# Performance work log

Hardware: AMD Instinct MI355X
Metric: run time of the kernel (lower is better)

## Reference

```python
import jax, jax.numpy as jnp
import numpy as np

B, N, C, H = 2, 2048, 768, 12
HD = C // H  # head dim = 64


def setup_inputs() -> dict:
    key = jax.random.key(0)
    k1, k2, k3 = jax.random.split(key, 3)
    x = jax.random.normal(k1, (B, N, C), dtype=jnp.float32)
    w_qkv = jax.random.normal(k2, (C, 3 * C), dtype=jnp.float32) * (C ** -0.5)
    w_proj = jax.random.normal(k3, (C, C), dtype=jnp.float32) * (C ** -0.5)
    b_proj = jnp.zeros((C,), dtype=jnp.float32)
    return {"x": x, "w_qkv": w_qkv, "w_proj": w_proj, "b_proj": b_proj}


def reference(x, w_qkv, w_proj, b_proj):
    scale = HD ** -0.5
    # qkv projection: [B,N,3C] -> [3,B,H,N,HD]
    qkv = (x @ w_qkv).reshape(B, N, 3, H, HD).transpose(2, 0, 3, 1, 4)
    q, k, v = qkv[0], qkv[1], qkv[2]
    # explicit QK^T softmax V (materializes [B,H,N,N] scores, as in source)
    attn = jnp.einsum("bhqd,bhkd->bhqk", q, k) * scale
    attn = jax.nn.softmax(attn, axis=-1)
    out = jnp.einsum("bhqk,bhkd->bhqd", attn, v)
    out = out.transpose(0, 2, 1, 3).reshape(B, N, C)
    return out @ w_proj + b_proj
```

## Files before the change

kernel.cpp:

```cpp
#include <hip/hip_runtime.h>

#define C_DIM 768
#define NSEQ 2048
#define H_DIM 12
#define HD 64
#define M_ROWS 4096
#define KSPLIT 2

typedef float f32x4 __attribute__((ext_vector_type(4)));
typedef short bf16x8 __attribute__((ext_vector_type(8)));
typedef _Float16 f16x8 __attribute__((ext_vector_type(8)));
typedef _Float16 f16x4 __attribute__((ext_vector_type(4)));
typedef __fp16 fp16x2 __attribute__((ext_vector_type(2)));
typedef __fp16 fp16x4 __attribute__((ext_vector_type(4)));
typedef __fp16 fp16x8 __attribute__((ext_vector_type(8)));
typedef unsigned short u16;

#define MFMA_PV(a, b, c) __builtin_amdgcn_mfma_f32_16x16x16f16(a, b, c, 0, 0, 0)

typedef unsigned int __attribute__((address_space(1))) as1_uint;
typedef unsigned int __attribute__((address_space(3))) as3_uint;
__device__ __forceinline__ void dma16(const void* g, void* l) {
  __builtin_amdgcn_global_load_lds((const as1_uint*)g, (as3_uint*)l, 16, 0, 0);
}

__device__ __forceinline__ u16 f2bf(float f) {
  union { float f; unsigned u; } v; v.f = f;
  unsigned u = v.u + 0x7FFFu + ((v.u >> 16) & 1u);
  return (u16)(u >> 16);
}

__global__ __launch_bounds__(256) void prep_kernel(const float* __restrict__ x,
                                                   const float* __restrict__ wq,
                                                   const float* __restrict__ wp,
                                                   u16* __restrict__ x_bf,
                                                   u16* __restrict__ outq,
                                                   __fp16* __restrict__ outp) {
  if (blockIdx.z == 2) {
    const int n4 = M_ROWS * C_DIM / 4;
    int lb = blockIdx.y * 72 + blockIdx.x;
    int i0 = lb * 256 + threadIdx.x;
    {
      float4 v = ((const float4*)x)[i0];
      ushort4 o;
      o.x = f2bf(v.x); o.y = f2bf(v.y); o.z = f2bf(v.z); o.w = f2bf(v.w);
      ((ushort4*)x_bf)[i0] = o;
    }
    int i1 = i0 + 442368;
    if (i1 < n4) {
      float4 v = ((const float4*)x)[i1];
      ushort4 o;
      o.x = f2bf(v.x); o.y = f2bf(v.y); o.z = f2bf(v.z); o.w = f2bf(v.w);
      ((ushort4*)x_bf)[i1] = o;
    }
    return;
  }
  const int R = C_DIM;
  __shared__ float t[32][33];
  int tx = threadIdx.x & 31, ty = threadIdx.x >> 5;
  int c0 = blockIdx.x * 32, r0 = blockIdx.y * 32;
  if (blockIdx.z == 0) {
    const int Cc = 3 * C_DIM;
#pragma unroll
    for (int i = 0; i < 4; i++)
      t[ty + i * 8][tx] = wq[(size_t)(r0 + ty + i * 8) * Cc + c0 + tx];
    __syncthreads();
#pragma unroll
    for (int i = 0; i < 4; i++)
      outq[(size_t)(c0 + ty + i * 8) * R + r0 + tx] = f2bf(t[tx][ty + i * 8]);
  } else {
    if (blockIdx.x >= 24) return;
    const int Cc = C_DIM;
#pragma unroll
    for (int i = 0; i < 4; i++)
      t[ty + i * 8][tx] = wp[(size_t)(r0 + ty + i * 8) * Cc + c0 + tx];
    __syncthreads();
#pragma unroll
    for (int i = 0; i < 4; i++)
      outp[(size_t)(c0 + ty + i * 8) * R + r0 + tx] = (__fp16)t[tx][ty + i * 8];
  }
}

__device__ __forceinline__ void gemm_core_128_db(const u16* __restrict__ A,
                                                 const u16* __restrict__ BT,
                                                 int m0, int n0,
                                                 u16 (*la)[128 * 32], u16 (*lb)[128 * 32],
                                                 f32x4 acc[4][4]) {
  const int K = C_DIM;
  int tid = threadIdx.x, lane = tid & 63, wave = tid >> 6;
  int wm = (wave >> 1) * 64, wn = (wave & 1) * 64;
  int quad = lane >> 4, l16 = lane & 15;

  int r0 = wave * 16 + (lane >> 2);
  int sw = (((lane & 3) ^ (r0 & 3)) * 8);
  const u16* ga0 = A + (size_t)(m0 + r0) * K + sw;
  const u16* ga1 = A + (size_t)(m0 + r0 + 64) * K + sw;
  const u16* gb0 = BT + (size_t)(n0 + r0) * K + sw;
  const u16* gb1 = BT + (size_t)(n0 + r0 + 64) * K + sw;
  int ofs0 = wave * 16 * 32, ofs1 = ofs0 + 64 * 32;

  dma16(ga0, la[0] + ofs0);
  dma16(ga1, la[0] + ofs1);
  dma16(gb0, lb[0] + ofs0);
  dma16(gb1, lb[0] + ofs1);

  const int NT = K / 32;
  for (int kt = 0; kt < NT; kt++) {
    int cur = kt & 1, nxt = cur ^ 1;
    __syncthreads();
    if (kt < NT - 1) {
      int k0 = (kt + 1) * 32;
      dma16(ga0 + k0, la[nxt] + ofs0);
      dma16(ga1 + k0, la[nxt] + ofs1);
      dma16(gb0 + k0, lb[nxt] + ofs0);
      dma16(gb1 + k0, lb[nxt] + ofs1);
    }
    bf16x8 af[4], bfr[4];
#pragma unroll
    for (int mt = 0; mt < 4; mt++) {
      int r = wm + mt * 16 + l16;
      af[mt] = *(const bf16x8*)(la[cur] + r * 32 + ((quad ^ (r & 3)) * 8));
    }
#pragma unroll
    for (int nt = 0; nt < 4; nt++) {
      int r = wn + nt * 16 + l16;
      bfr[nt] = *(const bf16x8*)(lb[cur] + r * 32 + ((quad ^ (r & 3)) * 8));
    }
#pragma unroll
    for (int mt = 0; mt < 4; mt++)
#pragma unroll
      for (int nt = 0; nt < 4; nt++)
        acc[mt][nt] = __builtin_amdgcn_mfma_f32_16x16x32_bf16(af[mt], bfr[nt], acc[mt][nt], 0, 0, 0);
  }
}

#define Q_PRESCALE 0.18033688011112042f
__global__ __launch_bounds__(256) void gemm_qkv_kernel(const u16* __restrict__ A,
                                                       const u16* __restrict__ BT,
                                                       _Float16* __restrict__ qb,
                                                       _Float16* __restrict__ kb,
                                                       _Float16* __restrict__ vtb) {
  __shared__ __align__(16) u16 la[2][128 * 32];
  __shared__ __align__(16) u16 lb[2][128 * 32];
  f32x4 acc[4][4] = {};
  int m0 = blockIdx.x * 128, n0 = blockIdx.y * 128;
  gemm_core_128_db(A, BT, m0, n0, la, lb, acc);

  int lane = threadIdx.x & 63, wave = threadIdx.x >> 6;
  int wm = (wave >> 1) * 64, wn = (wave & 1) * 64;
  int quad = lane >> 4, l16 = lane & 15;
#pragma unroll
  for (int mt = 0; mt < 4; mt++) {
#pragma unroll
    for (int nt = 0; nt < 4; nt++) {
      int gn = n0 + wn + nt * 16 + l16;
      int which = gn / C_DIM;
      int cc = gn - which * C_DIM;
      int h = cc >> 6, d = cc & 63;
      int gm0 = m0 + wm + mt * 16 + quad * 4;
      int b = gm0 >> 11, n = gm0 & 2047;
      size_t bh = (size_t)(b * H_DIM + h);
      if (which == 2) {
        f16x4 hv;
#pragma unroll
        for (int r = 0; r < 4; r++) hv[r] = (_Float16)acc[mt][nt][r];
        *(f16x4*)(vtb + (bh * HD + d) * NSEQ + n) = hv;
      } else if (which == 0) {
#pragma unroll
        for (int r = 0; r < 4; r++)
          qb[(bh * NSEQ + n + r) * HD + d] = (_Float16)(acc[mt][nt][r] * Q_PRESCALE);
      } else {
#pragma unroll
        for (int r = 0; r < 4; r++)
          kb[(bh * NSEQ + n + r) * HD + d] = (_Float16)acc[mt][nt][r];
      }
    }
  }
}

__global__ __launch_bounds__(256) void gemm_proj_kernel(const __fp16* __restrict__ opart,
                                                        const float* __restrict__ lpart,
                                                        const u16* __restrict__ BT,
                                                        const float* __restrict__ bias,
                                                        float* __restrict__ out) {
  __shared__ __align__(16) u16 la[2][64 * 32];
  __shared__ __align__(16) u16 lb[2][128 * 32];
  int tid = threadIdx.x, lane = tid & 63, wave = tid >> 6;
  int quad = lane >> 4, l16 = lane & 15;
  int wm = (wave >> 1) * 32, wn = (wave & 1) * 64;
  int m0 = blockIdx.x * 64, n0 = blockIdx.y * 128;

  int r0 = wave * 16 + (lane >> 2);
  int swb = (((lane & 3) ^ (r0 & 3)) * 8);
  const u16* gb0 = BT + (size_t)(n0 + r0) * C_DIM + swb;
  const u16* gb1 = BT + (size_t)(n0 + r0 + 64) * C_DIM + swb;
  int ofsB0 = wave * 16 * 32, ofsB1 = ofsB0 + 64 * 32;

  int ar = r0, cj = lane & 3;
  int m = m0 + ar;
  int bb = m >> 11, q = m & 2047;
  const __fp16* ap0 = opart + (size_t)m * C_DIM + cj * 8;
  const __fp16* ap1 = ap0 + (size_t)M_ROWS * C_DIM;
  int wslotA = ar * 32 + ((cj ^ (ar & 3)) * 8);

  f32x4 acc[2][4] = {};

  union pk_t { fp16x2 h2[4]; uint4 v; };

  dma16(gb0, lb[0] + ofsB0);
  dma16(gb1, lb[0] + ofsB1);
  {
    fp16x8 p0 = *(const fp16x8*)ap0;
    fp16x8 p1 = *(const fp16x8*)ap1;
    float l = lpart[((size_t)bb * H_DIM + 0) * NSEQ + q] +
              lpart[((size_t)(H_DIM * 2 + bb * H_DIM + 0)) * NSEQ + q];
    float inv = 1.f / l;
    pk_t w;
#pragma unroll
    for (int j = 0; j < 4; j++)
      w.h2[j] = __builtin_amdgcn_cvt_pkrtz(((float)p0[2 * j] + (float)p1[2 * j]) * inv,
                                           ((float)p0[2 * j + 1] + (float)p1[2 * j + 1]) * inv);
    *(uint4*)(la[0] + wslotA) = w.v;
  }

  const int NT = C_DIM / 32;
  for (int kt = 0; kt < NT; kt++) {
    int cur = kt & 1, nxt = cur ^ 1;
    __syncthreads();
    fp16x8 p0, p1;
    float inv = 0.f;
    if (kt < NT - 1) {
      int k0 = (kt + 1) * 32;
      dma16(gb0 + k0, lb[nxt] + ofsB0);
      dma16(gb1 + k0, lb[nxt] + ofsB1);
      p0 = *(const fp16x8*)(ap0 + k0);
      p1 = *(const fp16x8*)(ap1 + k0);
      int h = (kt + 1) >> 1;
      float l = lpart[((size_t)bb * H_DIM + h) * NSEQ + q] +
                lpart[((size_t)(H_DIM * 2 + bb * H_DIM + h)) * NSEQ + q];
      inv = 1.f / l;
    }
    f16x8 af[2], bf[4];
#pragma unroll
    for (int mt = 0; mt < 2; mt++) {
      int r = wm + mt * 16 + l16;
      af[mt] = *(const f16x8*)(la[cur] + r * 32 + ((quad ^ (r & 3)) * 8));
    }
#pragma unroll
    for (int nt = 0; nt < 4; nt++) {
      int r = wn + nt * 16 + l16;
      bf[nt] = *(const f16x8*)(lb[cur] + r * 32 + ((quad ^ (r & 3)) * 8));
    }
#pragma unroll
    for (int mt = 0; mt < 2; mt++)
#pragma unroll
      for (int nt = 0; nt < 4; nt++)
        acc[mt][nt] = __builtin_amdgcn_mfma_f32_16x16x32_f16(af[mt], bf[nt], acc[mt][nt], 0, 0, 0);
    if (kt < NT - 1) {
      pk_t w;
#pragma unroll
      for (int j = 0; j < 4; j++)
        w.h2[j] = __builtin_amdgcn_cvt_pkrtz(((float)p0[2 * j] + (float)p1[2 * j]) * inv,
                                             ((float)p0[2 * j + 1] + (float)p1[2 * j + 1]) * inv);
      *(uint4*)(la[nxt] + wslotA) = w.v;
    }
  }

#pragma unroll
  for (int mt = 0; mt < 2; mt++) {
#pragma unroll
    for (int nt = 0; nt < 4; nt++) {
      int gn = n0 + wn + nt * 16 + l16;
      float bv = bias[gn];
#pragma unroll
      for (int r = 0; r < 4; r++) {
        int gm = m0 + wm + mt * 16 + quad * 4 + r;
        out[(size_t)gm * C_DIM + gn] = acc[mt][nt][r] + bv;
      }
    }
  }
}

__global__ __launch_bounds__(256) void attn_kernel(const _Float16* __restrict__ qb,
                                                   const _Float16* __restrict__ kb,
                                                   const _Float16* __restrict__ vtb,
                                                   __fp16* __restrict__ opart,
                                                   float* __restrict__ lpart) {
  __shared__ __align__(16) u16 lk[2][64 * 72];
  __shared__ __align__(16) u16 lv[2][64 * 72];
  int bh = blockIdx.y, qblk = blockIdx.x, ks = blockIdx.z;
  int tid = threadIdx.x, lane = tid & 63, wave = tid >> 6;
  int quad = lane >> 4, l16 = lane & 15;

  const _Float16* q_bh = qb + (size_t)bh * NSEQ * HD;
  const u16* k_bh = (const u16*)(kb + (size_t)bh * NSEQ * HD);
  const u16* v_bh = (const u16*)(vtb + (size_t)bh * HD * NSEQ);

  int q0 = qblk * 128 + wave * 32 + l16;
  f16x8 qf[2][2];
#pragma unroll
  for (int qt = 0; qt < 2; qt++) {
    const _Float16* qp = q_bh + (size_t)(q0 + qt * 16) * HD + quad * 8;
    qf[qt][0] = *(const f16x8*)qp;
    qf[qt][1] = *(const f16x8*)(qp + 32);
  }

  f32x4 o[2][4] = {};
  float l_i[2] = {0.f, 0.f};

  int srow = tid >> 3, scj = tid & 7;
  const u16* kp0 = k_bh + (size_t)srow * HD + scj * 8;
  const u16* kp1 = kp0 + (size_t)32 * HD;
  const u16* vp0 = v_bh + (size_t)srow * NSEQ + scj * 8;
  const u16* vp1 = vp0 + (size_t)32 * NSEQ;
  int w0 = srow * 72 + scj * 8, w1 = (srow + 32) * 72 + scj * 8;

  const int kt_beg = ks * (NSEQ / 64 / KSPLIT);
  const int kt_end = kt_beg + (NSEQ / 64 / KSPLIT);

  {
    int k0 = kt_beg * 64;
    *(uint4*)(lk[0] + w0) = *(const uint4*)(kp0 + (size_t)k0 * HD);
    *(uint4*)(lk[0] + w1) = *(const uint4*)(kp1 + (size_t)k0 * HD);
    *(uint4*)(lv[0] + w0) = *(const uint4*)(vp0 + k0);
    *(uint4*)(lv[0] + w1) = *(const uint4*)(vp1 + k0);
  }

  for (int kt = kt_beg; kt < kt_end; kt++) {
    int cur = kt & 1, nxt = cur ^ 1;
    __syncthreads();

    uint4 rk0, rk1, rv0, rv1;
    if (kt < kt_end - 1) {
      int k0 = (kt + 1) * 64;
      rk0 = *(const uint4*)(kp0 + (size_t)k0 * HD);
      rk1 = *(const uint4*)(kp1 + (size_t)k0 * HD);
      rv0 = *(const uint4*)(vp0 + k0);
      rv1 = *(const uint4*)(vp1 + k0);
    }

    f32x4 s0[4], s1[4];
#pragma unroll
    for (int nt = 0; nt < 4; nt++) {
      const u16* kp = lk[cur] + (nt * 16 + l16) * 72 + quad * 8;
      f16x8 kf0 = *(const f16x8*)kp;
      f16x8 kf1 = *(const f16x8*)(kp + 32);
      f32x4 t0 = {}, t1 = {};
      t0 = __builtin_amdgcn_mfma_f32_16x16x32_f16(kf0, qf[0][0], t0, 0, 0, 0);
      t0 = __builtin_amdgcn_mfma_f32_16x16x32_f16(kf1, qf[0][1], t0, 0, 0, 0);
      t1 = __builtin_amdgcn_mfma_f32_16x16x32_f16(kf0, qf[1][0], t1, 0, 0, 0);
      t1 = __builtin_amdgcn_mfma_f32_16x16x32_f16(kf1, qf[1][1], t1, 0, 0, 0);
      s0[nt] = t0; s1[nt] = t1;
    }

#pragma unroll
    for (int nt = 0; nt < 4; nt++) {
      float a0 = __builtin_amdgcn_exp2f(s0[nt][0]);
      float a1 = __builtin_amdgcn_exp2f(s0[nt][1]);
      float a2 = __builtin_amdgcn_exp2f(s0[nt][2]);
      float a3 = __builtin_amdgcn_exp2f(s0[nt][3]);
      l_i[0] += (a0 + a1) + (a2 + a3);
      float b0 = __builtin_amdgcn_exp2f(s1[nt][0]);
      float b1 = __builtin_amdgcn_exp2f(s1[nt][1]);
      float b2 = __builtin_amdgcn_exp2f(s1[nt][2]);
      float b3 = __builtin_amdgcn_exp2f(s1[nt][3]);
      l_i[1] += (b0 + b1) + (b2 + b3);
      union { fp16x2 h2[2]; f16x4 h4; } pa, pb;
      pa.h2[0] = __builtin_amdgcn_cvt_pkrtz(a0, a1);
      pa.h2[1] = __builtin_amdgcn_cvt_pkrtz(a2, a3);
      pb.h2[0] = __builtin_amdgcn_cvt_pkrtz(b0, b1);
      pb.h2[1] = __builtin_amdgcn_cvt_pkrtz(b2, b3);
#pragma unroll
      for (int dt = 0; dt < 4; dt++) {
        f16x4 vf = *(const f16x4*)(lv[cur] + (dt * 16 + l16) * 72 + nt * 16 + quad * 4);
        o[0][dt] = MFMA_PV(vf, pa.h4, o[0][dt]);
        o[1][dt] = MFMA_PV(vf, pb.h4, o[1][dt]);
      }
    }

    if (kt < kt_end - 1) {
      *(uint4*)(lk[nxt] + w0) = rk0;
      *(uint4*)(lk[nxt] + w1) = rk1;
      *(uint4*)(lv[nxt] + w0) = rv0;
      *(uint4*)(lv[nxt] + w1) = rv1;
    }
  }

#pragma unroll
  for (int qt = 0; qt < 2; qt++) {
    l_i[qt] += __shfl_xor(l_i[qt], 16);
    l_i[qt] += __shfl_xor(l_i[qt], 32);
  }

  int b = bh / H_DIM, h = bh % H_DIM;
  __fp16* obase = opart + (size_t)ks * M_ROWS * C_DIM;
  float* lrow = lpart + ((size_t)ks * H_DIM * 2 + bh) * NSEQ;
#pragma unroll
  for (int qt = 0; qt < 2; qt++) {
    int q = q0 + qt * 16;
    if (quad == 0) lrow[q] = l_i[qt];
    __fp16* orow = obase + (size_t)(b * NSEQ + q) * C_DIM + h * HD;
#pragma unroll
    for (int dt = 0; dt < 4; dt++) {
      union { fp16x2 h2[2]; fp16x4 h4; } ov;
      ov.h2[0] = __builtin_amdgcn_cvt_pkrtz(o[qt][dt][0], o[qt][dt][1]);
      ov.h2[1] = __builtin_amdgcn_cvt_pkrtz(o[qt][dt][2], o[qt][dt][3]);
      *(fp16x4*)(orow + dt * 16 + quad * 4) = ov.h4;
    }
  }
}

extern "C" void kernel_launch(void* const* d_in, const int* in_sizes, int n_in,
                              void* d_out, int out_size, void* d_ws, size_t ws_size,
                              hipStream_t stream) {
  const float* x = (const float*)d_in[0];
  const float* w_qkv = (const float*)d_in[1];
  const float* w_proj = (const float*)d_in[2];
  const float* b_proj = (const float*)d_in[3];
  float* out = (float*)d_out;

  char* ws = (char*)d_ws;
  u16* x_bf        = (u16*)(ws);
  u16* wqkvT       = (u16*)(ws + 6291456);
  __fp16* wprojT   = (__fp16*)(ws + 9830400);
  _Float16* qb     = (_Float16*)(ws + 11010048);
  _Float16* kb     = (_Float16*)(ws + 17301504);
  _Float16* vtb    = (_Float16*)(ws + 23592960);
  __fp16* opart    = (__fp16*)(ws + 29884416);
  float* lpart     = (float*)(ws + 42467328);

  prep_kernel<<<dim3(72, 24, 3), 256, 0, stream>>>(x, w_qkv, w_proj, x_bf, wqkvT, wprojT);
  gemm_qkv_kernel<<<dim3(32, 18), 256, 0, stream>>>(x_bf, wqkvT, qb, kb, vtb);
  attn_kernel<<<dim3(16, 24, KSPLIT), 256, 0, stream>>>(qb, kb, vtb, opart, lpart);
  gemm_proj_kernel<<<dim3(64, 6), 256, 0, stream>>>(opart, lpart, (const u16*)wprojT,
                                                    b_proj, out);
}
```

Measured before the change: 162.1 us.

## Drop LDS staging in attention, widen query tile, raise key split to four

The attention kernel stops staging K and V through shared memory. Each lane now reads its MFMA fragments straight from global memory, which removes the barriers and the double buffering. Each wave now handles 64 queries instead of 32, so every K and V fragment is reused across more MFMAs, and the key dimension is split four ways to keep enough blocks in flight. The projection GEMM combines four partial outputs and row sums, which costs more partial-buffer traffic and a larger workspace. Direct global fragment loads depend on cache hits and use more registers.

```diff
diff --git a/kernel.cpp b/kernel.cpp
--- a/kernel.cpp
+++ b/kernel.cpp
@@ -5,7 +5,7 @@
 #define H_DIM 12
 #define HD 64
 #define M_ROWS 4096
-#define KSPLIT 2
+#define KSPLIT 4
 
 typedef float f32x4 __attribute__((ext_vector_type(4)));
 typedef short bf16x8 __attribute__((ext_vector_type(8)));
@@ -199,46 +199,41 @@
   int ar = r0, cj = lane & 3;
   int m = m0 + ar;
   int bb = m >> 11, q = m & 2047;
-  const __fp16* ap0 = opart + (size_t)m * C_DIM + cj * 8;
-  const __fp16* ap1 = ap0 + (size_t)M_ROWS * C_DIM;
+  const __fp16* ap = opart + (size_t)m * C_DIM + cj * 8;
   int wslotA = ar * 32 + ((cj ^ (ar & 3)) * 8);
 
   f32x4 acc[2][4] = {};
-
   union pk_t { fp16x2 h2[4]; uint4 v; };
+
+#define COMBINE_A(dstbuf, k0, hh)                                              \
+  {                                                                            \
+    float fs[8] = {0, 0, 0, 0, 0, 0, 0, 0};                                    \
+    float l = 0.f;                                                             \
+    _Pragma("unroll") for (int kk = 0; kk < KSPLIT; kk++) {                    \
+      fp16x8 pv = *(const fp16x8*)(ap + (size_t)kk * M_ROWS * C_DIM + (k0));   \
+      _Pragma("unroll") for (int j = 0; j < 8; j++) fs[j] += (float)pv[j];     \
+      l += lpart[((size_t)kk * H_DIM * 2 + bb * H_DIM + (hh)) * NSEQ + q];     \
+    }                                                                          \
+    float inv = 1.f / l;                                                       \
+    pk_t w;                                                                    \
+    _Pragma("unroll") for (int j = 0; j < 4; j++)                              \
+        w.h2[j] = __builtin_amdgcn_cvt_pkrtz(fs[2 * j] * inv, fs[2 * j + 1] * inv); \
+    *(uint4*)(la[dstbuf] + wslotA) = w.v;                                      \
+  }
 
   dma16(gb0, lb[0] + ofsB0);
   dma16(gb1, lb[0] + ofsB1);
-  {
-    fp16x8 p0 = *(const fp16x8*)ap0;
-    fp16x8 p1 = *(const fp16x8*)ap1;
-    float l = lpart[((size_t)bb * H_DIM + 0) * NSEQ + q] +
-              lpart[((size_t)(H_DIM * 2 + bb * H_DIM + 0)) * NSEQ + q];
-    float inv = 1.f / l;
-    pk_t w;
-#pragma unroll
-    for (int j = 0; j < 4; j++)
-      w.h2[j] = __builtin_amdgcn_cvt_pkrtz(((float)p0[2 * j] + (float)p1[2 * j]) * inv,
-                                           ((float)p0[2 * j + 1] + (float)p1[2 * j + 1]) * inv);
-    *(uint4*)(la[0] + wslotA) = w.v;
-  }
+  COMBINE_A(0, 0, 0);
 
   const int NT = C_DIM / 32;
   for (int kt = 0; kt < NT; kt++) {
     int cur = kt & 1, nxt = cur ^ 1;
     __syncthreads();
-    fp16x8 p0, p1;
-    float inv = 0.f;
     if (kt < NT - 1) {
       int k0 = (kt + 1) * 32;
       dma16(gb0 + k0, lb[nxt] + ofsB0);
       dma16(gb1 + k0, lb[nxt] + ofsB1);
-      p0 = *(const fp16x8*)(ap0 + k0);
-      p1 = *(const fp16x8*)(ap1 + k0);
-      int h = (kt + 1) >> 1;
-      float l = lpart[((size_t)bb * H_DIM + h) * NSEQ + q] +
-                lpart[((size_t)(H_DIM * 2 + bb * H_DIM + h)) * NSEQ + q];
-      inv = 1.f / l;
+      COMBINE_A(nxt, k0, (kt + 1) >> 1);
     }
     f16x8 af[2], bf[4];
 #pragma unroll
@@ -256,14 +251,6 @@
 #pragma unroll
       for (int nt = 0; nt < 4; nt++)
         acc[mt][nt] = __builtin_amdgcn_mfma_f32_16x16x32_f16(af[mt], bf[nt], acc[mt][nt], 0, 0, 0);
-    if (kt < NT - 1) {
-      pk_t w;
-#pragma unroll
-      for (int j = 0; j < 4; j++)
-        w.h2[j] = __builtin_amdgcn_cvt_pkrtz(((float)p0[2 * j] + (float)p1[2 * j]) * inv,
-                                             ((float)p0[2 * j + 1] + (float)p1[2 * j + 1]) * inv);
-      *(uint4*)(la[nxt] + wslotA) = w.v;
-    }
   }
 
 #pragma unroll
@@ -281,113 +268,80 @@
   }
 }
 
-__global__ __launch_bounds__(256) void attn_kernel(const _Float16* __restrict__ qb,
-                                                   const _Float16* __restrict__ kb,
-                                                   const _Float16* __restrict__ vtb,
-                                                   __fp16* __restrict__ opart,
-                                                   float* __restrict__ lpart) {
-  __shared__ __align__(16) u16 lk[2][64 * 72];
-  __shared__ __align__(16) u16 lv[2][64 * 72];
+__global__ __launch_bounds__(256, 3) void attn_kernel(const _Float16* __restrict__ qb,
+                                                      const _Float16* __restrict__ kb,
+                                                      const _Float16* __restrict__ vtb,
+                                                      __fp16* __restrict__ opart,
+                                                      float* __restrict__ lpart) {
   int bh = blockIdx.y, qblk = blockIdx.x, ks = blockIdx.z;
   int tid = threadIdx.x, lane = tid & 63, wave = tid >> 6;
   int quad = lane >> 4, l16 = lane & 15;
 
   const _Float16* q_bh = qb + (size_t)bh * NSEQ * HD;
-  const u16* k_bh = (const u16*)(kb + (size_t)bh * NSEQ * HD);
-  const u16* v_bh = (const u16*)(vtb + (size_t)bh * HD * NSEQ);
-
-  int q0 = qblk * 128 + wave * 32 + l16;
-  f16x8 qf[2][2];
-#pragma unroll
-  for (int qt = 0; qt < 2; qt++) {
+  const _Float16* k_bh = kb + (size_t)bh * NSEQ * HD;
+  const _Float16* v_bh = vtb + (size_t)bh * HD * NSEQ;
+
+  int q0 = qblk * 256 + wave * 64 + l16;
+  f16x8 qf[4][2];
+#pragma unroll
+  for (int qt = 0; qt < 4; qt++) {
     const _Float16* qp = q_bh + (size_t)(q0 + qt * 16) * HD + quad * 8;
     qf[qt][0] = *(const f16x8*)qp;
     qf[qt][1] = *(const f16x8*)(qp + 32);
   }
 
-  f32x4 o[2][4] = {};
-  float l_i[2] = {0.f, 0.f};
-
-  int srow = tid >> 3, scj = tid & 7;
-  const u16* kp0 = k_bh + (size_t)srow * HD + scj * 8;
-  const u16* kp1 = kp0 + (size_t)32 * HD;
-  const u16* vp0 = v_bh + (size_t)srow * NSEQ + scj * 8;
-  const u16* vp1 = vp0 + (size_t)32 * NSEQ;
-  int w0 = srow * 72 + scj * 8, w1 = (srow + 32) * 72 + scj * 8;
-
-  const int kt_beg = ks * (NSEQ / 64 / KSPLIT);
-  const int kt_end = kt_beg + (NSEQ / 64 / KSPLIT);
-
-  {
-    int k0 = kt_beg * 64;
-    *(uint4*)(lk[0] + w0) = *(const uint4*)(kp0 + (size_t)k0 * HD);
-    *(uint4*)(lk[0] + w1) = *(const uint4*)(kp1 + (size_t)k0 * HD);
-    *(uint4*)(lv[0] + w0) = *(const uint4*)(vp0 + k0);
-    *(uint4*)(lv[0] + w1) = *(const uint4*)(vp1 + k0);
-  }
-
-  for (int kt = kt_beg; kt < kt_end; kt++) {
-    int cur = kt & 1, nxt = cur ^ 1;
-    __syncthreads();
-
-    uint4 rk0, rk1, rv0, rv1;
-    if (kt < kt_end - 1) {
-      int k0 = (kt + 1) * 64;
-      rk0 = *(const uint4*)(kp0 + (size_t)k0 * HD);
-      rk1 = *(const uint4*)(kp1 + (size_t)k0 * HD);
-      rv0 = *(const uint4*)(vp0 + k0);
-      rv1 = *(const uint4*)(vp1 + k0);
-    }
-
-    f32x4 s0[4], s1[4];
-#pragma unroll
-    for (int nt = 0; nt < 4; nt++) {
-      const u16* kp = lk[cur] + (nt * 16 + l16) * 72 + quad * 8;
+  f32x4 o[4][4] = {};
+  float l_i[4] = {0.f, 0.f, 0.f, 0.f};
+
+  const int kbase = ks * (NSEQ / KSPLIT);
+  const _Float16* kR = k_bh + (size_t)(kbase + l16) * HD + quad * 8;
+  const _Float16* vB[4];
+#pragma unroll
+  for (int dt = 0; dt < 4; dt++)
+    vB[dt] = v_bh + (size_t)(dt * 16 + l16) * NSEQ + kbase + quad * 4;
+
+  const int NKT = NSEQ / 64 / KSPLIT;
+  for (int kt = 0; kt < NKT; kt++) {
+#pragma unroll
+    for (int nt = 0; nt < 4; nt++) {
+      int koff = kt * 64 + nt * 16;
+      const _Float16* kp = kR + (size_t)koff * HD;
       f16x8 kf0 = *(const f16x8*)kp;
       f16x8 kf1 = *(const f16x8*)(kp + 32);
-      f32x4 t0 = {}, t1 = {};
-      t0 = __builtin_amdgcn_mfma_f32_16x16x32_f16(kf0, qf[0][0], t0, 0, 0, 0);
-      t0 = __builtin_amdgcn_mfma_f32_16x16x32_f16(kf1, qf[0][1], t0, 0, 0, 0);
-      t1 = __builtin_amdgcn_mfma_f32_16x16x32_f16(kf0, qf[1][0], t1, 0, 0, 0);
-      t1 = __builtin_amdgcn_mfma_f32_16x16x32_f16(kf1, qf[1][1], t1, 0, 0, 0);
-      s0[nt] = t0; s1[nt] = t1;
-    }
-
-#pragma unroll
-    for (int nt = 0; nt < 4; nt++) {
-      float a0 = __builtin_amdgcn_exp2f(s0[nt][0]);
-      float a1 = __builtin_amdgcn_exp2f(s0[nt][1]);
-      float a2 = __builtin_amdgcn_exp2f(s0[nt][2]);
-      float a3 = __builtin_amdgcn_exp2f(s0[nt][3]);
-      l_i[0] += (a0 + a1) + (a2 + a3);
-      float b0 = __builtin_amdgcn_exp2f(s1[nt][0]);
-      float b1 = __builtin_amdgcn_exp2f(s1[nt][1]);
-      float b2 = __builtin_amdgcn_exp2f(s1[nt][2]);
-      float b3 = __builtin_amdgcn_exp2f(s1[nt][3]);
-      l_i[1] += (b0 + b1) + (b2 + b3);
-      union { fp16x2 h2[2]; f16x4 h4; } pa, pb;
-      pa.h2[0] = __builtin_amdgcn_cvt_pkrtz(a0, a1);
-      pa.h2[1] = __builtin_amdgcn_cvt_pkrtz(a2, a3);
-      pb.h2[0] = __builtin_amdgcn_cvt_pkrtz(b0, b1);
-      pb.h2[1] = __builtin_amdgcn_cvt_pkrtz(b2, b3);
-#pragma unroll
-      for (int dt = 0; dt < 4; dt++) {
-        f16x4 vf = *(const f16x4*)(lv[cur] + (dt * 16 + l16) * 72 + nt * 16 + quad * 4);
-        o[0][dt] = MFMA_PV(vf, pa.h4, o[0][dt]);
-        o[1][dt] = MFMA_PV(vf, pb.h4, o[1][dt]);
+      f16x4 vf[4];
+#pragma unroll
+      for (int dt = 0; dt < 4; dt++) vf[dt] = *(const f16x4*)(vB[dt] + koff);
+      f32x4 s[4];
+#pragma unroll
+      for (int qt = 0; qt < 4; qt++) {
+        f32x4 t = {};
+        t = __builtin_amdgcn_mfma_f32_16x16x32_f16(kf0, qf[qt][0], t, 0, 0, 0);
+        t = __builtin_amdgcn_mfma_f32_16x16x32_f16(kf1, qf[qt][1], t, 0, 0, 0);
+        s[qt] = t;
       }
-    }
-
-    if (kt < kt_end - 1) {
-      *(uint4*)(lk[nxt] + w0) = rk0;
-      *(uint4*)(lk[nxt] + w1) = rk1;
-      *(uint4*)(lv[nxt] + w0) = rv0;
-      *(uint4*)(lv[nxt] + w1) = rv1;
-    }
-  }
-
-#pragma unroll
-  for (int qt = 0; qt < 2; qt++) {
+      f16x4 p[4];
+#pragma unroll
+      for (int qt = 0; qt < 4; qt++) {
+        float e0 = __builtin_amdgcn_exp2f(s[qt][0]);
+        float e1 = __builtin_amdgcn_exp2f(s[qt][1]);
+        float e2 = __builtin_amdgcn_exp2f(s[qt][2]);
+        float e3 = __builtin_amdgcn_exp2f(s[qt][3]);
+        l_i[qt] += (e0 + e1) + (e2 + e3);
+        union { fp16x2 h2[2]; f16x4 h4; } u;
+        u.h2[0] = __builtin_amdgcn_cvt_pkrtz(e0, e1);
+        u.h2[1] = __builtin_amdgcn_cvt_pkrtz(e2, e3);
+        p[qt] = u.h4;
+      }
+#pragma unroll
+      for (int dt = 0; dt < 4; dt++)
+#pragma unroll
+        for (int qt = 0; qt < 4; qt++)
+          o[qt][dt] = MFMA_PV(vf[dt], p[qt], o[qt][dt]);
+    }
+  }
+
+#pragma unroll
+  for (int qt = 0; qt < 4; qt++) {
     l_i[qt] += __shfl_xor(l_i[qt], 16);
     l_i[qt] += __shfl_xor(l_i[qt], 32);
   }
@@ -396,7 +350,7 @@
   __fp16* obase = opart + (size_t)ks * M_ROWS * C_DIM;
   float* lrow = lpart + ((size_t)ks * H_DIM * 2 + bh) * NSEQ;
 #pragma unroll
-  for (int qt = 0; qt < 2; qt++) {
+  for (int qt = 0; qt < 4; qt++) {
     int q = q0 + qt * 16;
     if (quad == 0) lrow[q] = l_i[qt];
     __fp16* orow = obase + (size_t)(b * NSEQ + q) * C_DIM + h * HD;
@@ -427,11 +381,11 @@
   _Float16* kb     = (_Float16*)(ws + 17301504);
   _Float16* vtb    = (_Float16*)(ws + 23592960);
   __fp16* opart    = (__fp16*)(ws + 29884416);
-  float* lpart     = (float*)(ws + 42467328);
+  float* lpart     = (float*)(ws + 55050240);
 
   prep_kernel<<<dim3(72, 24, 3), 256, 0, stream>>>(x, w_qkv, w_proj, x_bf, wqkvT, wprojT);
   gemm_qkv_kernel<<<dim3(32, 18), 256, 0, stream>>>(x_bf, wqkvT, qb, kb, vtb);
-  attn_kernel<<<dim3(16, 24, KSPLIT), 256, 0, stream>>>(qb, kb, vtb, opart, lpart);
+  attn_kernel<<<dim3(8, 24, KSPLIT), 256, 0, stream>>>(qb, kb, vtb, opart, lpart);
   gemm_proj_kernel<<<dim3(64, 6), 256, 0, stream>>>(opart, lpart, (const u16*)wprojT,
                                                     b_proj, out);
 }
```

New measurement: 259.5 us. +60.0%, slower.

## Transpose MFMA accumulator layout for vector epilogue stores and repad attention LDS

Applied to the files above, without the earlier changes.

The MFMA operands in the QKV and projection GEMMs are swapped, so each lane holds four consecutive output columns instead of four rows. The Q and K stores become 8-byte vector stores and the projection output becomes float4 stores with a float4 bias load. The cost is that the transposed V store turns into scalar strided writes. The projection kernel now combines its A split-K parts before the MFMAs through a macro generalised over KSPLIT, and the attention LDS row pitch changes from 72 to 76 halves to alter bank mapping. With that pitch, 16-byte LDS accesses on odd rows are no longer 16-byte aligned.

```diff
diff --git a/kernel.cpp b/kernel.cpp
--- a/kernel.cpp
+++ b/kernel.cpp
@@ -6,6 +6,7 @@
 #define HD 64
 #define M_ROWS 4096
 #define KSPLIT 2
+#define PADK 76
 
 typedef float f32x4 __attribute__((ext_vector_type(4)));
 typedef short bf16x8 __attribute__((ext_vector_type(8)));
@@ -130,7 +131,7 @@
     for (int mt = 0; mt < 4; mt++)
 #pragma unroll
       for (int nt = 0; nt < 4; nt++)
-        acc[mt][nt] = __builtin_amdgcn_mfma_f32_16x16x32_bf16(af[mt], bfr[nt], acc[mt][nt], 0, 0, 0);
+        acc[mt][nt] = __builtin_amdgcn_mfma_f32_16x16x32_bf16(bfr[nt], af[mt], acc[mt][nt], 0, 0, 0);
   }
 }
 
@@ -153,26 +154,27 @@
   for (int mt = 0; mt < 4; mt++) {
 #pragma unroll
     for (int nt = 0; nt < 4; nt++) {
-      int gn = n0 + wn + nt * 16 + l16;
-      int which = gn / C_DIM;
-      int cc = gn - which * C_DIM;
-      int h = cc >> 6, d = cc & 63;
-      int gm0 = m0 + wm + mt * 16 + quad * 4;
-      int b = gm0 >> 11, n = gm0 & 2047;
+      int gm = m0 + wm + mt * 16 + l16;
+      int b = gm >> 11, n = gm & 2047;
+      int gn0 = n0 + wn + nt * 16 + quad * 4;
+      int which = gn0 / C_DIM;
+      int cc = gn0 - which * C_DIM;
+      int h = cc >> 6, d0 = cc & 63;
       size_t bh = (size_t)(b * H_DIM + h);
       if (which == 2) {
+#pragma unroll
+        for (int r = 0; r < 4; r++)
+          vtb[(bh * HD + d0 + r) * NSEQ + n] = (_Float16)acc[mt][nt][r];
+      } else if (which == 0) {
         f16x4 hv;
 #pragma unroll
+        for (int r = 0; r < 4; r++) hv[r] = (_Float16)(acc[mt][nt][r] * Q_PRESCALE);
+        *(f16x4*)(qb + (bh * NSEQ + n) * HD + d0) = hv;
+      } else {
+        f16x4 hv;
+#pragma unroll
         for (int r = 0; r < 4; r++) hv[r] = (_Float16)acc[mt][nt][r];
-        *(f16x4*)(vtb + (bh * HD + d) * NSEQ + n) = hv;
-      } else if (which == 0) {
-#pragma unroll
-        for (int r = 0; r < 4; r++)
-          qb[(bh * NSEQ + n + r) * HD + d] = (_Float16)(acc[mt][nt][r] * Q_PRESCALE);
-      } else {
-#pragma unroll
-        for (int r = 0; r < 4; r++)
-          kb[(bh * NSEQ + n + r) * HD + d] = (_Float16)acc[mt][nt][r];
+        *(f16x4*)(kb + (bh * NSEQ + n) * HD + d0) = hv;
       }
     }
   }
@@ -199,46 +201,41 @@
   int ar = r0, cj = lane & 3;
   int m = m0 + ar;
   int bb = m >> 11, q = m & 2047;
-  const __fp16* ap0 = opart + (size_t)m * C_DIM + cj * 8;
-  const __fp16* ap1 = ap0 + (size_t)M_ROWS * C_DIM;
+  const __fp16* ap = opart + (size_t)m * C_DIM + cj * 8;
   int wslotA = ar * 32 + ((cj ^ (ar & 3)) * 8);
 
   f32x4 acc[2][4] = {};
-
   union pk_t { fp16x2 h2[4]; uint4 v; };
+
+#define COMBINE_A(dstbuf, k0, hh)                                              \
+  {                                                                            \
+    float fs[8] = {0, 0, 0, 0, 0, 0, 0, 0};                                    \
+    float l = 0.f;                                                             \
+    _Pragma("unroll") for (int kk = 0; kk < KSPLIT; kk++) {                    \
+      fp16x8 pv = *(const fp16x8*)(ap + (size_t)kk * M_ROWS * C_DIM + (k0));   \
+      _Pragma("unroll") for (int j = 0; j < 8; j++) fs[j] += (float)pv[j];     \
+      l += lpart[((size_t)kk * H_DIM * 2 + bb * H_DIM + (hh)) * NSEQ + q];     \
+    }                                                                          \
+    float inv = 1.f / l;                                                       \
+    pk_t w;                                                                    \
+    _Pragma("unroll") for (int j = 0; j < 4; j++)                              \
+        w.h2[j] = __builtin_amdgcn_cvt_pkrtz(fs[2 * j] * inv, fs[2 * j + 1] * inv); \
+    *(uint4*)(la[dstbuf] + wslotA) = w.v;                                      \
+  }
 
   dma16(gb0, lb[0] + ofsB0);
   dma16(gb1, lb[0] + ofsB1);
-  {
-    fp16x8 p0 = *(const fp16x8*)ap0;
-    fp16x8 p1 = *(const fp16x8*)ap1;
-    float l = lpart[((size_t)bb * H_DIM + 0) * NSEQ + q] +
-              lpart[((size_t)(H_DIM * 2 + bb * H_DIM + 0)) * NSEQ + q];
-    float inv = 1.f / l;
-    pk_t w;
-#pragma unroll
-    for (int j = 0; j < 4; j++)
-      w.h2[j] = __builtin_amdgcn_cvt_pkrtz(((float)p0[2 * j] + (float)p1[2 * j]) * inv,
-                                           ((float)p0[2 * j + 1] + (float)p1[2 * j + 1]) * inv);
-    *(uint4*)(la[0] + wslotA) = w.v;
-  }
+  COMBINE_A(0, 0, 0);
 
   const int NT = C_DIM / 32;
   for (int kt = 0; kt < NT; kt++) {
     int cur = kt & 1, nxt = cur ^ 1;
     __syncthreads();
-    fp16x8 p0, p1;
-    float inv = 0.f;
     if (kt < NT - 1) {
       int k0 = (kt + 1) * 32;
       dma16(gb0 + k0, lb[nxt] + ofsB0);
       dma16(gb1 + k0, lb[nxt] + ofsB1);
-      p0 = *(const fp16x8*)(ap0 + k0);
-      p1 = *(const fp16x8*)(ap1 + k0);
-      int h = (kt + 1) >> 1;
-      float l = lpart[((size_t)bb * H_DIM + h) * NSEQ + q] +
-                lpart[((size_t)(H_DIM * 2 + bb * H_DIM + h)) * NSEQ + q];
-      inv = 1.f / l;
+      COMBINE_A(nxt, k0, (kt + 1) >> 1);
     }
     f16x8 af[2], bf[4];
 #pragma unroll
@@ -255,28 +252,22 @@
     for (int mt = 0; mt < 2; mt++)
 #pragma unroll
       for (int nt = 0; nt < 4; nt++)
-        acc[mt][nt] = __builtin_amdgcn_mfma_f32_16x16x32_f16(af[mt], bf[nt], acc[mt][nt], 0, 0, 0);
-    if (kt < NT - 1) {
-      pk_t w;
-#pragma unroll
-      for (int j = 0; j < 4; j++)
-        w.h2[j] = __builtin_amdgcn_cvt_pkrtz(((float)p0[2 * j] + (float)p1[2 * j]) * inv,
-                                             ((float)p0[2 * j + 1] + (float)p1[2 * j + 1]) * inv);
-      *(uint4*)(la[nxt] + wslotA) = w.v;
-    }
+        acc[mt][nt] = __builtin_amdgcn_mfma_f32_16x16x32_f16(bf[nt], af[mt], acc[mt][nt], 0, 0, 0);
   }
 
 #pragma unroll
   for (int mt = 0; mt < 2; mt++) {
 #pragma unroll
     for (int nt = 0; nt < 4; nt++) {
-      int gn = n0 + wn + nt * 16 + l16;
-      float bv = bias[gn];
-#pragma unroll
-      for (int r = 0; r < 4; r++) {
-        int gm = m0 + wm + mt * 16 + quad * 4 + r;
-        out[(size_t)gm * C_DIM + gn] = acc[mt][nt][r] + bv;
-      }
+      int gm = m0 + wm + mt * 16 + l16;
+      int gn0 = n0 + wn + nt * 16 + quad * 4;
+      float4 bv = *(const float4*)(bias + gn0);
+      float4 o4;
+      o4.x = acc[mt][nt][0] + bv.x;
+      o4.y = acc[mt][nt][1] + bv.y;
+      o4.z = acc[mt][nt][2] + bv.z;
+      o4.w = acc[mt][nt][3] + bv.w;
+      *(float4*)(out + (size_t)gm * C_DIM + gn0) = o4;
     }
   }
 }
@@ -286,8 +277,8 @@
                                                    const _Float16* __restrict__ vtb,
                                                    __fp16* __restrict__ opart,
                                                    float* __restrict__ lpart) {
-  __shared__ __align__(16) u16 lk[2][64 * 72];
-  __shared__ __align__(16) u16 lv[2][64 * 72];
+  __shared__ __align__(16) u16 lk[2][64 * PADK];
+  __shared__ __align__(16) u16 lv[2][64 * PADK];
   int bh = blockIdx.y, qblk = blockIdx.x, ks = blockIdx.z;
   int tid = threadIdx.x, lane = tid & 63, wave = tid >> 6;
   int quad = lane >> 4, l16 = lane & 15;
@@ -313,7 +304,7 @@
   const u16* kp1 = kp0 + (size_t)32 * HD;
   const u16* vp0 = v_bh + (size_t)srow * NSEQ + scj * 8;
   const u16* vp1 = vp0 + (size_t)32 * NSEQ;
-  int w0 = srow * 72 + scj * 8, w1 = (srow + 32) * 72 + scj * 8;
+  int w0 = srow * PADK + scj * 8, w1 = (srow + 32) * PADK + scj * 8;
 
   const int kt_beg = ks * (NSEQ / 64 / KSPLIT);
   const int kt_end = kt_beg + (NSEQ / 64 / KSPLIT);
@@ -342,7 +333,7 @@
     f32x4 s0[4], s1[4];
 #pragma unroll
     for (int nt = 0; nt < 4; nt++) {
-      const u16* kp = lk[cur] + (nt * 16 + l16) * 72 + quad * 8;
+      const u16* kp = lk[cur] + (nt * 16 + l16) * PADK + quad * 8;
       f16x8 kf0 = *(const f16x8*)kp;
       f16x8 kf1 = *(const f16x8*)(kp + 32);
       f32x4 t0 = {}, t1 = {};
@@ -372,7 +363,7 @@
       pb.h2[1] = __builtin_amdgcn_cvt_pkrtz(b2, b3);
 #pragma unroll
       for (int dt = 0; dt < 4; dt++) {
-        f16x4 vf = *(const f16x4*)(lv[cur] + (dt * 16 + l16) * 72 + nt * 16 + quad * 4);
+        f16x4 vf = *(const f16x4*)(lv[cur] + (dt * 16 + l16) * PADK + nt * 16 + quad * 4);
         o[0][dt] = MFMA_PV(vf, pa.h4, o[0][dt]);
         o[1][dt] = MFMA_PV(vf, pb.h4, o[1][dt]);
       }
```

Result: slower. 191.3 us (+18.0%).
